# Optimization experiments

Hardware: AMD Instinct MI355X
Metric: run time of the kernel (lower is better)

The kernel has to match this reference:

```python
import jax, jax.numpy as jnp
import numpy as np

EMBED = 512
HEADS = 8
HEAD_DIM = EMBED // HEADS
EPS = 1e-5


def setup_inputs() -> dict:
    key = jax.random.key(0)
    ks = jax.random.split(key, 10)
    s = 1.0 / np.sqrt(EMBED)
    x = jax.random.normal(ks[0], (2, 4096, EMBED), dtype=jnp.float32)
    Wq = jax.random.uniform(ks[1], (EMBED, EMBED), jnp.float32, -s, s)
    bq = jnp.zeros((EMBED,), jnp.float32)
    Wk = jax.random.uniform(ks[2], (EMBED, EMBED), jnp.float32, -s, s)
    bk = jnp.zeros((EMBED,), jnp.float32)
    Wv = jax.random.uniform(ks[3], (EMBED, EMBED), jnp.float32, -s, s)
    bv = jnp.zeros((EMBED,), jnp.float32)
    Wo = jax.random.uniform(ks[4], (EMBED, EMBED), jnp.float32, -s, s)
    bo = jnp.zeros((EMBED,), jnp.float32)
    gamma = jnp.ones((EMBED,), jnp.float32)
    beta = jnp.zeros((EMBED,), jnp.float32)
    return {"x": x, "Wq": Wq, "bq": bq, "Wk": Wk, "bk": bk,
            "Wv": Wv, "bv": bv, "Wo": Wo, "bo": bo,
            "gamma": gamma, "beta": beta}


def reference(x, Wq, bq, Wk, bk, Wv, bv, Wo, bo, gamma, beta):
    b, n, e = x.shape
    def split_heads(t):  # [b,n,e] -> [b,h,n,d]
        return t.reshape(b, n, HEADS, HEAD_DIM).transpose(0, 2, 1, 3)
    q = split_heads(x @ Wq + bq)
    k = split_heads(x @ Wk + bk)
    v = split_heads(x @ Wv + bv)
    energy = jnp.einsum('bhqd,bhkd->bhqk', q, k) * (HEAD_DIM ** -0.5)
    attn = jax.nn.softmax(energy, axis=-1)  # dropout=0.0 (eval)
    out = jnp.einsum('bhqk,bhkd->bhqd', attn, v)
    out = out.transpose(0, 2, 1, 3).reshape(b, n, e)
    out = out @ Wo + bo
    y = x + out
    mu = jnp.mean(y, axis=-1, keepdims=True)
    var = jnp.var(y, axis=-1, keepdims=True)
    return (y - mu) * jax.lax.rsqrt(var + EPS) * gamma + beta
```

## Files before the change

### kernel.cpp

```cpp
#include <hip/hip_runtime.h>
#include <hip/hip_bf16.h>


#define ROWS 8192
#define EMB  512
#define SEQ  4096
#define HEADS 8
#define HD   64
#define QSCALE 0.18033688011112042f

typedef __attribute__((ext_vector_type(8))) short bf16x8;
typedef __attribute__((ext_vector_type(4))) short bf16x4;
typedef __attribute__((ext_vector_type(4))) float f32x4;

#define MFMA_K16(A, B, C) __builtin_amdgcn_mfma_f32_16x16x16bf16_1k(A, B, C, 0, 0, 0)

__device__ __forceinline__ float bf16_to_f(unsigned short u) {
    union { unsigned int i; float f; } v; v.i = ((unsigned int)u) << 16; return v.f;
}
__device__ __forceinline__ unsigned short f_to_bf16(float f) {
    union { __hip_bfloat16 h; unsigned short u; } v; v.h = __float2bfloat16(f); return v.u;
}
__device__ __forceinline__ unsigned int pack_bf16_trunc(float a, float b) {
    return (__float_as_uint(a) >> 16) | (__float_as_uint(b) & 0xFFFF0000u);
}
__device__ __forceinline__ void load_lds16(const void* g, void* l) {
    __builtin_amdgcn_global_load_lds(
        (const __attribute__((address_space(1))) void*)g,
        (__attribute__((address_space(3))) void*)l, 16, 0, 0);
}

__global__ void detect_kernel(const void* x, int* flag) {
    const unsigned short* p = (const unsigned short*)x;
    int t = threadIdx.x;
    int cnt = 0;
    for (int i = 0; i < 4; ++i) {
        unsigned short u = p[t * 4 + i];
        int e = (u >> 7) & 0xFF;
        if (e >= 140) cnt++;
    }
    for (int off = 32; off > 0; off >>= 1) cnt += __shfl_down(cnt, off, 64);
    if (t == 0) *flag = (cnt > 16) ? 1 : 0;
}

__global__ __launch_bounds__(256) void conv_x_kernel(const void* __restrict__ x,
        unsigned short* __restrict__ xb, const int* __restrict__ flag) {
    if (*flag == 0) return;
    int i = (blockIdx.x * 256 + threadIdx.x) * 4;
    float4 v = *(const float4*)((const float*)x + i);
    ushort4 u = { f_to_bf16(v.x), f_to_bf16(v.y), f_to_bf16(v.z), f_to_bf16(v.w) };
    *(ushort4*)(xb + i) = u;
}

__global__ __launch_bounds__(256) void conv_wt_kernel(
        const void* W0, const void* W1, const void* W2, const void* W3,
        unsigned short* __restrict__ Wt, const int* __restrict__ flag) {
    __shared__ float T[64][65];
    int tid = threadIdx.x;
    int kt = blockIdx.x, nt = blockIdx.y, mat = blockIdx.z;
    const void* src = (mat == 0) ? W0 : (mat == 1) ? W1 : (mat == 2) ? W2 : W3;
    int fp32 = *flag;
    for (int ii = 0; ii < 4; ++ii) {
        int idx = tid + ii * 256;
        int i = idx >> 4, j = (idx & 15) * 4;
        size_t g = (size_t)(kt * 64 + i) * 512 + nt * 64 + j;
        if (fp32) {
            float4 v = *(const float4*)((const float*)src + g);
            T[i][j] = v.x; T[i][j+1] = v.y; T[i][j+2] = v.z; T[i][j+3] = v.w;
        } else {
            ushort4 u = *(const ushort4*)((const unsigned short*)src + g);
            T[i][j] = bf16_to_f(u.x); T[i][j+1] = bf16_to_f(u.y);
            T[i][j+2] = bf16_to_f(u.z); T[i][j+3] = bf16_to_f(u.w);
        }
    }
    __syncthreads();
    for (int ii = 0; ii < 2; ++ii) {
        int idx = tid + ii * 256;
        int j = idx >> 3, ch = idx & 7;
        unsigned short pk[8];
        for (int t = 0; t < 8; ++t) pk[t] = f_to_bf16(T[ch * 8 + t][j]);
        *(bf16x8*)&Wt[(size_t)(mat * 512 + nt * 64 + j) * 512 + kt * 64 + ch * 8] = *(bf16x8*)pk;
    }
}

__global__ __launch_bounds__(256) void conv_small_kernel(
        const void* b0, const void* b1, const void* b2, const void* b3,
        const void* b4, const void* b5, float* __restrict__ dst, const int* __restrict__ flag) {
    int idx = blockIdx.x * 256 + threadIdx.x;
    int mat = idx >> 9, off = idx & 511;
    const void* src = (mat == 0) ? b0 : (mat == 1) ? b1 : (mat == 2) ? b2 :
                      (mat == 3) ? b3 : (mat == 4) ? b4 : b5;
    float v;
    if (*flag) v = ((const float*)src)[off];
    else       v = bf16_to_f(((const unsigned short*)src)[off]);
    dst[idx] = v;
}

template <typename OutT>
__global__ __launch_bounds__(256) void gemm_mfma_kernel(
        const unsigned short* __restrict__ A_conv, const unsigned short* __restrict__ A_raw,
        const int* __restrict__ flag,
        const unsigned short* __restrict__ Bt,
        const float* __restrict__ bias, OutT* __restrict__ C, int ldc, int scale_cols,
        unsigned short* __restrict__ VtOut) {
    __shared__ unsigned short At[128 * 64];
    __shared__ unsigned short Bs[128 * 64];
    const unsigned short* A = (*flag) ? A_conv : A_raw;
    int tid = threadIdx.x;
    int wave = tid >> 6, lane = tid & 63;
    int l15 = lane & 15, quad = lane >> 4;

    int lin = blockIdx.x + gridDim.x * blockIdx.y;
    int nwg = gridDim.x * gridDim.y;
    int bx, by;
    if (nwg & 7) { bx = blockIdx.x; by = blockIdx.y; }
    else {
        int t = (lin & 7) * (nwg >> 3) + (lin >> 3);
        bx = t % gridDim.x; by = t / gridDim.x;
    }
    int m0 = by * 128, n0 = bx * 128;
    int wm = (wave & 1) * 64, wn = (wave >> 1) * 64;

    int rt = wave * 32 + (lane >> 3);
    int ch = (lane & 7) ^ ((lane >> 3) & 7);
    const unsigned short* ag = A  + (size_t)(m0 + rt) * 512 + ch * 8;
    const unsigned short* bg = Bt + (size_t)(n0 + rt) * 512 + ch * 8;

    f32x4 acc[4][4];
    for (int i = 0; i < 4; ++i) for (int j = 0; j < 4; ++j) acc[i][j] = (f32x4){0.f,0.f,0.f,0.f};

    for (int k0 = 0; k0 < 512; k0 += 64) {
        __syncthreads();
        #pragma unroll
        for (int j = 0; j < 4; ++j) {
            load_lds16(ag + (size_t)(j * 8) * 512 + k0, &At[(wave * 32 + j * 8) * 64]);
            load_lds16(bg + (size_t)(j * 8) * 512 + k0, &Bs[(wave * 32 + j * 8) * 64]);
        }
        __syncthreads();
        #pragma unroll
        for (int ks = 0; ks < 2; ++ks) {
            bf16x8 a[4], b[4];
            #pragma unroll
            for (int f = 0; f < 4; ++f) {
                int pc = ((ks * 4 + quad) ^ (l15 & 7)) * 8;
                a[f] = *(const bf16x8*)&At[(wm + f * 16 + l15) * 64 + pc];
                b[f] = *(const bf16x8*)&Bs[(wn + f * 16 + l15) * 64 + pc];
            }
            #pragma unroll
            for (int fm = 0; fm < 4; ++fm)
                #pragma unroll
                for (int fn = 0; fn < 4; ++fn)
                    acc[fm][fn] = __builtin_amdgcn_mfma_f32_16x16x32_bf16(a[fm], b[fn], acc[fm][fn], 0, 0, 0);
        }
    }
    #pragma unroll
    for (int fm = 0; fm < 4; ++fm) {
        #pragma unroll
        for (int fn = 0; fn < 4; ++fn) {
            int col = n0 + wn + fn * 16 + l15;
            float bia = bias[col];
            float sc = (col < scale_cols) ? QSCALE : 1.f;
            int rowbase = m0 + wm + fm * 16 + quad * 4;
            float v0 = (acc[fm][fn][0] + bia) * sc;
            float v1 = (acc[fm][fn][1] + bia) * sc;
            float v2 = (acc[fm][fn][2] + bia) * sc;
            float v3 = (acc[fm][fn][3] + bia) * sc;
            if (VtOut && col >= 1024) {
                int hd = col - 1024;
                int bh = (rowbase >> 12) * 8 + (hd >> 6);
                int d  = hd & 63;
                ushort4 pk = { f_to_bf16(v0), f_to_bf16(v1), f_to_bf16(v2), f_to_bf16(v3) };
                *(ushort4*)&VtOut[((size_t)(bh * 64 + d)) * SEQ + (rowbase & 4095)] = pk;
            } else {
                if constexpr (sizeof(OutT) == 2) {
                    C[(size_t)(rowbase + 0) * ldc + col] = (OutT)f_to_bf16(v0);
                    C[(size_t)(rowbase + 1) * ldc + col] = (OutT)f_to_bf16(v1);
                    C[(size_t)(rowbase + 2) * ldc + col] = (OutT)f_to_bf16(v2);
                    C[(size_t)(rowbase + 3) * ldc + col] = (OutT)f_to_bf16(v3);
                } else {
                    C[(size_t)(rowbase + 0) * ldc + col] = v0;
                    C[(size_t)(rowbase + 1) * ldc + col] = v1;
                    C[(size_t)(rowbase + 2) * ldc + col] = v2;
                    C[(size_t)(rowbase + 3) * ldc + col] = v3;
                }
            }
        }
    }
}

__global__ __launch_bounds__(256, 4) void attn_kernel(
        const unsigned short* __restrict__ QKV, const unsigned short* __restrict__ Vt,
        unsigned short* __restrict__ Ab) {
    __shared__ __align__(16) unsigned char smem[32768];
    float* Ored = (float*)smem;
    float* Lred = (float*)(smem + 16384);

    int tid = threadIdx.x;
    int wave = tid >> 6, lane = tid & 63;
    int l15 = lane & 15, quad = lane >> 4;
    int qh = wave >> 1, kh = wave & 1;
    int lin = blockIdx.x;
    int xcd = lin & 7, slot = lin >> 3;
    int grp = xcd + 8 * (slot >> 6);
    int qt = slot & 63;
    int h = grp & 7, b = grp >> 3;
    int bh = b * HEADS + h;
    size_t qrow0 = (size_t)b * SEQ + qt * 64;

    bf16x8 aq[2][2];
    #pragma unroll
    for (int t = 0; t < 2; ++t) {
        const unsigned short* qp = &QKV[(qrow0 + qh * 32 + t * 16 + l15) * 1536 + h * 64];
        aq[t][0] = *(const bf16x8*)&qp[quad * 8];
        aq[t][1] = *(const bf16x8*)&qp[32 + quad * 8];
    }
    f32x4 o[2][4];
    #pragma unroll
    for (int t = 0; t < 2; ++t)
        #pragma unroll
        for (int db = 0; db < 4; ++db) o[t][db] = (f32x4){0.f, 0.f, 0.f, 0.f};
    float lp[2] = {0.f, 0.f};

    int r8 = lane >> 3;
    int kch = (lane & 7) ^ (r8 & 7);
    const unsigned short* kg = &QKV[((size_t)b * SEQ + r8) * 1536 + 512 + h * 64 + kch * 8];
    const unsigned short* vg = &Vt[((size_t)bh * 64 + wave * 16 + r8) * SEQ + kch * 8];

#define STAGE(buf, kt2) do {                                                          \
        unsigned short* Ksb = (unsigned short*)(smem + (buf) * 8192);                 \
        unsigned short* Vsb = (unsigned short*)(smem + 16384 + (buf) * 8192);         \
        load_lds16(kg + (size_t)((kt2) * 64 + wave * 16) * 1536,                      \
                   &Ksb[(wave * 16) * 64]);                                           \
        load_lds16(kg + (size_t)((kt2) * 64 + wave * 16 + 8) * 1536,                  \
                   &Ksb[(wave * 16 + 8) * 64]);                                       \
        load_lds16(vg + (size_t)((kt2) * 64), &Vsb[(wave * 16) * 64]);                \
        load_lds16(vg + (size_t)((kt2) * 64) + (size_t)8 * SEQ,                       \
                   &Vsb[(wave * 16 + 8) * 64]);                                       \
    } while (0)

    STAGE(0, 0);

    for (int kt = 0; kt < SEQ / 64; ++kt) {
        int cur = kt & 1;
        asm volatile("s_waitcnt vmcnt(0)" ::: "memory");
        __builtin_amdgcn_sched_barrier(0);
        asm volatile("s_barrier" ::: "memory");
        __builtin_amdgcn_sched_barrier(0);
        if (kt + 1 < SEQ / 64) STAGE(cur ^ 1, kt + 1);

        const unsigned short* Ksc = (const unsigned short*)(smem + cur * 8192);
        const unsigned short* Vsc = (const unsigned short*)(smem + 16384 + cur * 8192);
        #pragma unroll
        for (int nb = 0; nb < 2; ++nb) {
            int kc = kh * 32 + nb * 16;
            int krow = kc + l15;
            int key = krow & 7;
            bf16x8 kA0 = *(const bf16x8*)&Ksc[krow * 64 + (quad ^ key) * 8];
            bf16x8 kA1 = *(const bf16x8*)&Ksc[krow * 64 + ((4 + quad) ^ key) * 8];
            bf16x4 bv[4];
            #pragma unroll
            for (int db = 0; db < 4; ++db) {
                int d = db * 16 + l15;
                int c16 = (kc >> 3) + (quad >> 1);
                int sub = (quad & 1) * 4;
                bv[db] = *(const bf16x4*)&Vsc[d * 64 + ((c16 ^ (d & 7)) * 8) + sub];
            }
            #pragma unroll
            for (int t = 0; t < 2; ++t) {
                f32x4 sv = {0.f, 0.f, 0.f, 0.f};
                sv = __builtin_amdgcn_mfma_f32_16x16x32_bf16(kA0, aq[t][0], sv, 0, 0, 0);
                sv = __builtin_amdgcn_mfma_f32_16x16x32_bf16(kA1, aq[t][1], sv, 0, 0, 0);
                float p0 = __builtin_amdgcn_exp2f(sv[0]);
                float p1 = __builtin_amdgcn_exp2f(sv[1]);
                float p2 = __builtin_amdgcn_exp2f(sv[2]);
                float p3 = __builtin_amdgcn_exp2f(sv[3]);
                lp[t] += (p0 + p1) + (p2 + p3);
                union { unsigned int u[2]; bf16x4 v; } ap;
                ap.u[0] = pack_bf16_trunc(p0, p1);
                ap.u[1] = pack_bf16_trunc(p2, p3);
                #pragma unroll
                for (int db = 0; db < 4; ++db)
                    o[t][db] = MFMA_K16(ap.v, bv[db], o[t][db]);
            }
        }
        __builtin_amdgcn_sched_barrier(0);
    }
#undef STAGE

    __syncthreads();
    #pragma unroll
    for (int t = 0; t < 2; ++t) {
        float v = lp[t];
        v += __shfl_xor(v, 16, 64);
        v += __shfl_xor(v, 32, 64);
        if (quad == 0) Lred[(wave * 2 + t) * 16 + l15] = v;
    }
    __syncthreads();
    float* myO = Ored + wave * (16 * 64);
    #pragma unroll
    for (int t = 0; t < 2; ++t) {
        #pragma unroll
        for (int db = 0; db < 4; ++db)
            #pragma unroll
            for (int r = 0; r < 4; ++r)
                myO[(quad * 4 + r) * 64 + db * 16 + l15] = o[t][db][r];
        __syncthreads();
        {
            int q_l = tid >> 3;
            int dg = tid & 7;
            int qh2 = q_l >> 4, qq = q_l & 15;
            const float* r0 = Ored + (qh2 * 2 + 0) * (16 * 64) + qq * 64 + dg * 8;
            const float* r1 = Ored + (qh2 * 2 + 1) * (16 * 64) + qq * 64 + dg * 8;
            float4 a0 = *(const float4*)&r0[0];
            float4 a1 = *(const float4*)&r0[4];
            float4 c0 = *(const float4*)&r1[0];
            float4 c1 = *(const float4*)&r1[4];
            float lt = Lred[((qh2 * 2 + 0) * 2 + t) * 16 + qq] +
                       Lred[((qh2 * 2 + 1) * 2 + t) * 16 + qq];
            float inv = 1.f / lt;
            size_t row = qrow0 + qh2 * 32 + t * 16 + qq;
            unsigned short* dst = &Ab[row * EMB + h * 64 + dg * 8];
            ushort4 lo = { f_to_bf16((a0.x + c0.x) * inv), f_to_bf16((a0.y + c0.y) * inv),
                           f_to_bf16((a0.z + c0.z) * inv), f_to_bf16((a0.w + c0.w) * inv) };
            ushort4 hi = { f_to_bf16((a1.x + c1.x) * inv), f_to_bf16((a1.y + c1.y) * inv),
                           f_to_bf16((a1.z + c1.z) * inv), f_to_bf16((a1.w + c1.w) * inv) };
            *(ushort4*)&dst[0] = lo;
            *(ushort4*)&dst[4] = hi;
        }
        __syncthreads();
    }
}

__global__ __launch_bounds__(256) void ln_kernel(
        const float* __restrict__ xf, const unsigned short* __restrict__ xraw,
        const unsigned short* __restrict__ P,
        const float* __restrict__ gamma, const float* __restrict__ beta,
        void* __restrict__ out, const int* __restrict__ flag) {
    int row = blockIdx.x * 4 + (threadIdx.x >> 6);
    int t = threadIdx.x & 63;
    int fp32 = *flag;
    float v[8];
    float s = 0.f, ss = 0.f;
    const unsigned short* pp = &P[(size_t)row * EMB + t * 8];
    ushort4 p0 = *(const ushort4*)&pp[0];
    ushort4 p1 = *(const ushort4*)&pp[4];
    float pv[8] = { bf16_to_f(p0.x), bf16_to_f(p0.y), bf16_to_f(p0.z), bf16_to_f(p0.w),
                    bf16_to_f(p1.x), bf16_to_f(p1.y), bf16_to_f(p1.z), bf16_to_f(p1.w) };
    if (fp32) {
        const float* xp = &xf[(size_t)row * EMB + t * 8];
        for (int i = 0; i < 8; i += 4) {
            float4 x4 = *(const float4*)&xp[i];
            v[i] = x4.x + pv[i]; v[i+1] = x4.y + pv[i+1];
            v[i+2] = x4.z + pv[i+2]; v[i+3] = x4.w + pv[i+3];
        }
    } else {
        const unsigned short* xp = &xraw[(size_t)row * EMB + t * 8];
        ushort4 x0 = *(const ushort4*)&xp[0];
        ushort4 x1 = *(const ushort4*)&xp[4];
        v[0] = bf16_to_f(x0.x) + pv[0]; v[1] = bf16_to_f(x0.y) + pv[1];
        v[2] = bf16_to_f(x0.z) + pv[2]; v[3] = bf16_to_f(x0.w) + pv[3];
        v[4] = bf16_to_f(x1.x) + pv[4]; v[5] = bf16_to_f(x1.y) + pv[5];
        v[6] = bf16_to_f(x1.z) + pv[6]; v[7] = bf16_to_f(x1.w) + pv[7];
    }
    for (int i = 0; i < 8; ++i) { s += v[i]; ss += v[i] * v[i]; }
    for (int off = 32; off > 0; off >>= 1) {
        s  += __shfl_xor(s, off, 64);
        ss += __shfl_xor(ss, off, 64);
    }
    float mu = s * (1.f / 512.f);
    float var = ss * (1.f / 512.f) - mu * mu;
    float rs = rsqrtf(var + 1e-5f);
    for (int i = 0; i < 8; ++i) {
        int col = t * 8 + i;
        float y = (v[i] - mu) * rs * gamma[col] + beta[col];
        if (fp32) ((float*)out)[(size_t)row * EMB + col] = y;
        else      ((__hip_bfloat16*)out)[(size_t)row * EMB + col] = __float2bfloat16(y);
    }
}

extern "C" void kernel_launch(void* const* d_in, const int* in_sizes, int n_in,
                              void* d_out, int out_size, void* d_ws, size_t ws_size,
                              hipStream_t stream) {
    char* ws = (char*)d_ws;
    int* flag = (int*)ws;
    char* p = ws + 256;
    float* bias_all = (float*)p;       p += 6 * 512 * 4;
    unsigned short* Wt   = (unsigned short*)p; p += (size_t)2048 * 512 * 2;
    unsigned short* QKVb = (unsigned short*)p; p += (size_t)ROWS * 1536 * 2;
    unsigned short* Vt   = (unsigned short*)p; p += (size_t)16 * HD * SEQ * 2;
    unsigned short* xb = (unsigned short*)p;
    unsigned short* Ab = (unsigned short*)p;   p += (size_t)ROWS * EMB * 2;
    unsigned short* Pb = (unsigned short*)p;   p += (size_t)ROWS * EMB * 2;

    detect_kernel<<<1, 64, 0, stream>>>(d_in[0], flag);

    conv_x_kernel<<<ROWS * EMB / 1024, 256, 0, stream>>>(d_in[0], xb, flag);
    conv_wt_kernel<<<dim3(8, 8, 4), 256, 0, stream>>>(d_in[1], d_in[3], d_in[5], d_in[7], Wt, flag);
    conv_small_kernel<<<12, 256, 0, stream>>>(d_in[2], d_in[4], d_in[6], d_in[8], d_in[9], d_in[10],
                                              bias_all, flag);

    gemm_mfma_kernel<unsigned short><<<dim3(12, 64), 256, 0, stream>>>(
        xb, (const unsigned short*)d_in[0], flag, Wt, bias_all, QKVb, 1536, 512, Vt);

    attn_kernel<<<dim3(1024), 256, 0, stream>>>(QKVb, Vt, Ab);

    gemm_mfma_kernel<unsigned short><<<dim3(4, 64), 256, 0, stream>>>(
        Ab, Ab, flag, Wt + (size_t)1536 * 512, bias_all + 1536, Pb, 512, 0,
        (unsigned short*)nullptr);

    ln_kernel<<<ROWS / 4, 256, 0, stream>>>((const float*)d_in[0],
                                            (const unsigned short*)d_in[0], Pb,
                                            bias_all + 4 * 512, bias_all + 5 * 512, d_out, flag);
}
```

Measured before the change: 245.5 us.

## Double-buffer GEMM LDS tiles, use perm for bf16 pack, raise MFMA priority

The projection GEMM now keeps two LDS buffers and prefetches the next K tile with global_load_lds while the MFMAs run on the current one. This replaces the two barriers per K step with a single waitcnt plus barrier. In the attention kernel, the bf16 truncation-pack uses a single v_perm instead of a shift, mask and or, and s_setprio raises wave priority around the MFMA groups so they interleave better with exp work from other waves. The cost is double the GEMM LDS footprint (64KB), which may lower occupancy.

Measured after the change: 238.0 us. 1.03x faster.

```diff
diff --git a/kernel.cpp b/kernel.cpp
--- a/kernel.cpp
+++ b/kernel.cpp
@@ -22,7 +22,7 @@
     union { __hip_bfloat16 h; unsigned short u; } v; v.h = __float2bfloat16(f); return v.u;
 }
 __device__ __forceinline__ unsigned int pack_bf16_trunc(float a, float b) {
-    return (__float_as_uint(a) >> 16) | (__float_as_uint(b) & 0xFFFF0000u);
+    return __builtin_amdgcn_perm(__float_as_uint(b), __float_as_uint(a), 0x07060302u);
 }
 __device__ __forceinline__ void load_lds16(const void* g, void* l) {
     __builtin_amdgcn_global_load_lds(
@@ -103,8 +103,7 @@
         const unsigned short* __restrict__ Bt,
         const float* __restrict__ bias, OutT* __restrict__ C, int ldc, int scale_cols,
         unsigned short* __restrict__ VtOut) {
-    __shared__ unsigned short At[128 * 64];
-    __shared__ unsigned short Bs[128 * 64];
+    __shared__ __align__(16) unsigned short smemg[2][2][128 * 64];
     const unsigned short* A = (*flag) ? A_conv : A_raw;
     int tid = threadIdx.x;
     int wave = tid >> 6, lane = tid & 63;
@@ -129,14 +128,28 @@
     f32x4 acc[4][4];
     for (int i = 0; i < 4; ++i) for (int j = 0; j < 4; ++j) acc[i][j] = (f32x4){0.f,0.f,0.f,0.f};
 
-    for (int k0 = 0; k0 < 512; k0 += 64) {
-        __syncthreads();
-        #pragma unroll
-        for (int j = 0; j < 4; ++j) {
-            load_lds16(ag + (size_t)(j * 8) * 512 + k0, &At[(wave * 32 + j * 8) * 64]);
-            load_lds16(bg + (size_t)(j * 8) * 512 + k0, &Bs[(wave * 32 + j * 8) * 64]);
-        }
-        __syncthreads();
+#define GSTAGE(buf, k0) do {                                                      \
+        unsigned short* Atb = &smemg[buf][0][0];                                  \
+        unsigned short* Bsb = &smemg[buf][1][0];                                  \
+        _Pragma("unroll")                                                         \
+        for (int j = 0; j < 4; ++j) {                                             \
+            load_lds16(ag + (size_t)(j * 8) * 512 + (k0), &Atb[(wave * 32 + j * 8) * 64]); \
+            load_lds16(bg + (size_t)(j * 8) * 512 + (k0), &Bsb[(wave * 32 + j * 8) * 64]); \
+        }                                                                         \
+    } while (0)
+
+    GSTAGE(0, 0);
+
+    for (int s = 0; s < 8; ++s) {
+        int cur = s & 1;
+        asm volatile("s_waitcnt vmcnt(0)" ::: "memory");
+        __builtin_amdgcn_sched_barrier(0);
+        asm volatile("s_barrier" ::: "memory");
+        __builtin_amdgcn_sched_barrier(0);
+        if (s + 1 < 8) GSTAGE(cur ^ 1, (s + 1) * 64);
+
+        const unsigned short* At = &smemg[cur][0][0];
+        const unsigned short* Bs = &smemg[cur][1][0];
         #pragma unroll
         for (int ks = 0; ks < 2; ++ks) {
             bf16x8 a[4], b[4];
@@ -152,7 +165,10 @@
                 for (int fn = 0; fn < 4; ++fn)
                     acc[fm][fn] = __builtin_amdgcn_mfma_f32_16x16x32_bf16(a[fm], b[fn], acc[fm][fn], 0, 0, 0);
         }
-    }
+        __builtin_amdgcn_sched_barrier(0);
+    }
+#undef GSTAGE
+
     #pragma unroll
     for (int fm = 0; fm < 4; ++fm) {
         #pragma unroll
@@ -268,8 +284,10 @@
             #pragma unroll
             for (int t = 0; t < 2; ++t) {
                 f32x4 sv = {0.f, 0.f, 0.f, 0.f};
+                __builtin_amdgcn_s_setprio(1);
                 sv = __builtin_amdgcn_mfma_f32_16x16x32_bf16(kA0, aq[t][0], sv, 0, 0, 0);
                 sv = __builtin_amdgcn_mfma_f32_16x16x32_bf16(kA1, aq[t][1], sv, 0, 0, 0);
+                __builtin_amdgcn_s_setprio(0);
                 float p0 = __builtin_amdgcn_exp2f(sv[0]);
                 float p1 = __builtin_amdgcn_exp2f(sv[1]);
                 float p2 = __builtin_amdgcn_exp2f(sv[2]);
@@ -278,9 +296,11 @@
                 union { unsigned int u[2]; bf16x4 v; } ap;
                 ap.u[0] = pack_bf16_trunc(p0, p1);
                 ap.u[1] = pack_bf16_trunc(p2, p3);
+                __builtin_amdgcn_s_setprio(1);
                 #pragma unroll
                 for (int db = 0; db < 4; ++db)
                     o[t][db] = MFMA_K16(ap.v, bv[db], o[t][db]);
+                __builtin_amdgcn_s_setprio(0);
             }
         }
         __builtin_amdgcn_sched_barrier(0);
```
